# Performance work log

Hardware: AMD Instinct MI355X
Metric: run time of the kernel (lower is better)

The kernel has to match this reference:

```python
import jax, jax.numpy as jnp
import numpy as np
import math

B, S, DM = 32, 512, 1024   # batch (= groups*channels), seq_len, d_model
H, D, C = 16, 64, 8        # n_heads, d_kv, n_channels
NB, MD = 32, 128           # relative_attention_num_buckets, max_distance


def setup_inputs() -> dict:
    key = jax.random.key(0)
    ks = jax.random.split(key, 7)
    return {
        "hidden_states": jax.random.normal(ks[0], (B, S, DM), jnp.float32),
        "Wq": jax.random.normal(ks[1], (DM, H * D), jnp.float32) * 0.02,
        "Wk": jax.random.normal(ks[2], (DM, H * D), jnp.float32) * 0.02,
        "Wv": jax.random.normal(ks[3], (DM, H * D), jnp.float32) * 0.02,
        "Wo": jax.random.normal(ks[4], (H * D, DM), jnp.float32) * 0.02,
        "rel_emb": jax.random.normal(ks[5], (NB, H), jnp.float32) * 0.02,
        "beta": jax.random.normal(ks[6], (1, 1, H, 1, 1), jnp.float32) * 0.01,
    }


def _rel_bucket(relative_position, num_buckets=NB, max_distance=MD):
    # bidirectional (encoder) bucketing, faithful to T5
    nb = num_buckets // 2
    buckets = (relative_position > 0).astype(jnp.int32) * nb
    rp = jnp.abs(relative_position)
    max_exact = nb // 2
    is_small = rp < max_exact
    rp_safe = jnp.maximum(rp, 1).astype(jnp.float32)
    large = max_exact + (
        jnp.log(rp_safe / max_exact) / math.log(max_distance / max_exact) * (nb - max_exact)
    ).astype(jnp.int32)
    large = jnp.minimum(large, nb - 1)
    return buckets + jnp.where(is_small, rp, large)


def reference(hidden_states, Wq, Wk, Wv, Wo, rel_emb, beta):
    G = B // C  # groups

    def proj(W):
        # (B,S,DM) -> (B,S,H,D) -> (B,H,S,D) -> (G,C,H,S,D)
        x = (hidden_states @ W).reshape(B, S, H, D).transpose(0, 2, 1, 3)
        return x.reshape(G, C, H, S, D)

    q, k, v = proj(Wq), proj(Wk), proj(Wv)

    # relative position bias: (1,1,H,S,S)
    rel_pos = jnp.arange(S)[None, :] - jnp.arange(S)[:, None]
    bias = rel_emb[_rel_bucket(rel_pos)].transpose(2, 0, 1)[None, None]

    # local (dot-product) attention, T5-style: no 1/sqrt(d) scaling
    scores = jnp.einsum('gchsd,gchtd->gchst', q, k) + bias
    attn_w = jax.nn.softmax(scores, axis=-1)
    a_dot = jnp.einsum('gchst,gchtd->gchsd', attn_w, v)

    # compressive memory: ELU+1 feature map, summed over channels
    sk = jax.nn.elu(k) + 1.0
    M = jnp.einsum('gchsd,gchse->ghde', sk, v)   # (G,H,D,D)
    z = sk.sum(axis=3).sum(axis=1)               # (G,H,D)
    sq = jax.nn.elu(q) + 1.0
    num = jnp.einsum('gchsd,ghde->gchse', sq, M)
    den = jnp.einsum('gchsd,ghd->gchs', sq, z)[..., None] + 1e-6
    a_mem = num / den

    gate = jax.nn.sigmoid(beta)  # (1,1,H,1,1)
    out = gate * a_mem + (1.0 - gate) * a_dot

    # (G,C,H,S,D) -> (B,H,S,D) -> (B,S,H*D)
    out = out.reshape(B, H, S, D).transpose(0, 2, 1, 3).reshape(B, S, H * D)
    return out @ Wo
```

## Files before the change

### kernel.cpp

```cpp
#include <hip/hip_runtime.h>
#include <stdint.h>

typedef unsigned short u16;
typedef u16 u16x8 __attribute__((ext_vector_type(8)));
typedef u16 u16x4 __attribute__((ext_vector_type(4)));
typedef __bf16 bf16x8 __attribute__((ext_vector_type(8)));
typedef float f32x4 __attribute__((ext_vector_type(4)));

#define DEV static __device__ __forceinline__

DEV u16 f2bf(float f) {
  union { float f; uint32_t u; } v; v.f = f;
  uint32_t r = v.u + 0x7FFFu + ((v.u >> 16) & 1u);
  return (u16)(r >> 16);
}
DEV float bf2f(u16 s) {
  union { uint32_t u; float f; } v; v.u = ((uint32_t)s) << 16;
  return v.f;
}
DEV float elu1(float x) { return x > 0.f ? x + 1.f : __expf(x); }
DEV u16x8 ld8u(const u16* p) { return *reinterpret_cast<const u16x8*>(p); }

DEV f32x4 mfma16(u16x8 a, u16x8 b, f32x4 c) {
  return __builtin_amdgcn_mfma_f32_16x16x32_bf16(
      __builtin_bit_cast(bf16x8, a), __builtin_bit_cast(bf16x8, b), c, 0, 0, 0);
}
DEV void async16(void* lds, const void* g) {
  __builtin_amdgcn_global_load_lds(
      (__attribute__((address_space(1))) void*)g,
      (__attribute__((address_space(3))) void*)lds, 16, 0, 0);
}

#define BARR __builtin_amdgcn_s_barrier()
#define LG0  asm volatile("s_waitcnt lgkmcnt(0)" ::: "memory")
#define VMC(N) asm volatile("s_waitcnt vmcnt(" #N ")" ::: "memory")


__global__ __launch_bounds__(1024) void k_prep(const float* __restrict__ hs,
                                               const float* __restrict__ Wq, const float* __restrict__ Wk,
                                               const float* __restrict__ Wv, const float* __restrict__ Wo,
                                               const float* __restrict__ rel,
                                               u16* __restrict__ hsb, u16* __restrict__ wt,
                                               u16* __restrict__ wot, float* __restrict__ bias) {
  __shared__ float tb[32][33];
  const int blk = blockIdx.x;
  if (blk < 2048) {
    int i = blk * 1024 + threadIdx.x;
    const float4* p = reinterpret_cast<const float4*>(hs) + (size_t)i * 2;
    float4 a = p[0], bq = p[1];
    u16x8 o;
    o[0] = f2bf(a.x); o[1] = f2bf(a.y); o[2] = f2bf(a.z); o[3] = f2bf(a.w);
    o[4] = f2bf(bq.x); o[5] = f2bf(bq.y); o[6] = f2bf(bq.z); o[7] = f2bf(bq.w);
    reinterpret_cast<u16x8*>(hsb)[i] = o;
  } else if (blk < 6144) {
    const int bid2 = blk - 2048;
    int mat = bid2 >> 10;
    int tile = bid2 & 1023;
    int n0 = (tile >> 5) * 32;
    int k0 = (tile & 31) * 32;
    const float* W = (mat == 0) ? Wq : (mat == 1) ? Wk : (mat == 2) ? Wv : Wo;
    int tx = threadIdx.x & 31, ty = threadIdx.x >> 5;
    tb[ty][tx] = W[(size_t)(k0 + ty) * 1024 + n0 + tx];
    __syncthreads();
    u16 v = f2bf(tb[tx][ty]);
    if (mat < 3) wt[(size_t)(mat * 1024 + n0 + ty) * 1024 + k0 + tx] = v;
    else         wot[(size_t)(n0 + ty) * 1024 + k0 + tx] = v;
  } else {
    int off = threadIdx.x;
    if (off < 1023) {
      int rp = off - 511;
      int bck = rp > 0 ? 16 : 0;
      int arp = rp < 0 ? -rp : rp;
      int idx;
      if (arp < 8) idx = arp;
      else {
        float l = logf((float)arp * 0.125f) / logf(16.0f) * 8.0f;
        int lg = 8 + (int)l;
        idx = lg < 15 ? lg : 15;
      }
      bck += idx;
      for (int h = 0; h < 16; ++h) bias[h * 1023 + off] = rel[bck * 16 + h];
    }
  }
}


template <int EPI>
__global__ __launch_bounds__(512, 3) void k_g256(const u16* __restrict__ A, const u16* __restrict__ Bt,
                                                 u16* __restrict__ oq, u16* __restrict__ ok2,
                                                 u16* __restrict__ ovt, float* __restrict__ of) {
  __shared__ __align__(16) u16 lsA[2][128 * 32];
  __shared__ __align__(16) u16 lsB[2][256 * 32];
  const int t = threadIdx.x;
  const int lane = t & 63, w = t >> 6;
  const int wm = w >> 2, wn = w & 3;
  const int lr = lane & 15, lg = lane >> 4;

  const int bid = blockIdx.x;
  const int xcd = bid & 7, local = bid >> 3;
  const int s = local >> 4, w16 = local & 15;
  const int msq = s & 3, nsq = s >> 2;
  const int m0 = (xcd * 16 + msq * 4 + (w16 >> 2)) * 128;
  const int n0 = (nsq * 4 + (w16 & 3)) * 256;

  auto stage = [&](int kt, int slot) {
    const int k0 = kt * 32;
    {
      int c = t, S = c >> 3, q = (c & 7) ^ (S & 7);
      int row = 2 * S + (q >> 2), u = q & 3;
      async16(&lsA[slot][c * 8], A + (size_t)(m0 + row) * 1024 + k0 + u * 8);
    }
#pragma unroll
    for (int i = 0; i < 2; ++i) {
      int c = i * 512 + t, S = c >> 3, q = (c & 7) ^ (S & 7);
      int row = 2 * S + (q >> 2), u = q & 3;
      async16(&lsB[slot][c * 8], Bt + (size_t)(n0 + row) * 1024 + k0 + u * 8);
    }
  };
  auto rdoff = [&](int r_) -> int {
    return (r_ >> 1) * 64 + (((((r_ & 1) << 2) + lg) ^ ((r_ >> 1) & 7)) << 3);
  };

  f32x4 acc[4][4];
#pragma unroll
  for (int i = 0; i < 4; ++i)
#pragma unroll
    for (int j = 0; j < 4; ++j) acc[i][j] = (f32x4){0.f, 0.f, 0.f, 0.f};

  stage(0, 0);
  stage(1, 1);
  VMC(3);
  BARR;

  for (int kt = 0; kt < 32; ++kt) {
    const int slot = kt & 1;
    const u16* la = &lsA[slot][0];
    const u16* lb = &lsB[slot][0];

    u16x8 af[4], bf[4];
#pragma unroll
    for (int mi = 0; mi < 4; ++mi) af[mi] = ld8u(la + rdoff(wm * 64 + mi * 16 + lr));
#pragma unroll
    for (int ni = 0; ni < 4; ++ni) bf[ni] = ld8u(lb + rdoff(wn * 64 + ni * 16 + lr));
    LG0;
    BARR;
    if (kt + 2 < 32) stage(kt + 2, slot);

    __builtin_amdgcn_s_setprio(1);
#pragma unroll
    for (int mi = 0; mi < 4; ++mi)
#pragma unroll
      for (int ni = 0; ni < 4; ++ni)
        acc[mi][ni] = mfma16(af[mi], bf[ni], acc[mi][ni]);
    __builtin_amdgcn_s_setprio(0);

    if (kt + 2 < 32)      { VMC(3); }
    else if (kt == 30)    { VMC(0); }
    BARR;
  }

  if (EPI == 0) {
    const int which = n0 >> 10;
    const int nb = (n0 & 1023) + wn * 64;
#pragma unroll
    for (int mi = 0; mi < 4; ++mi)
#pragma unroll
      for (int r = 0; r < 4; ++r) {
        int m = m0 + wm * 64 + mi * 16 + lg * 4 + r;
        int b = m >> 9, s2 = m & 511;
#pragma unroll
        for (int ni = 0; ni < 4; ++ni) {
          int nc = nb + ni * 16 + lr;
          int h = nc >> 6, d = nc & 63;
          int bh = b * 16 + h;
          u16 v = f2bf(acc[mi][ni][r]);
          if (which == 0)      oq[(size_t)(bh * 512 + s2) * 64 + d] = v;
          else if (which == 1) ok2[(size_t)(bh * 512 + s2) * 64 + d] = v;
          else                 ovt[(size_t)(bh * 64 + d) * 512 + s2] = v;
        }
      }
  } else {
#pragma unroll
    for (int mi = 0; mi < 4; ++mi)
#pragma unroll
      for (int r = 0; r < 4; ++r) {
        int m = m0 + wm * 64 + mi * 16 + lg * 4 + r;
#pragma unroll
        for (int ni = 0; ni < 4; ++ni) {
          int n = n0 + wn * 64 + ni * 16 + lr;
          of[(size_t)m * 1024 + n] = acc[mi][ni][r];
        }
      }
  }
}


__global__ __launch_bounds__(256) void k_mem(const u16* __restrict__ K, const u16* __restrict__ Vt,
                                             float* __restrict__ Mp, float* __restrict__ zp) {
  __shared__ __align__(16) u16 skT[64 * 128];
  __shared__ __align__(16) u16 lV[64 * 128];
  __shared__ float mbuf[64][65];
  __shared__ float zsh[4][64];
  const int bid = blockIdx.x;
  const int g = bid >> 7, h = (bid >> 3) & 15, c = bid & 7;
  const int bh = (g * 8 + c) * 16 + h;
  const u16* kp = K + (size_t)bh * 512 * 64;
  const u16* vp = Vt + (size_t)bh * 64 * 512;
  const int t = threadIdx.x, lane = t & 63, w = t >> 6;
  const int lr = lane & 15, lg = lane >> 4;
  const int dmy = t & 63, sq = t >> 6;

  f32x4 acc[4][4];
#pragma unroll
  for (int i = 0; i < 4; ++i)
#pragma unroll
    for (int j = 0; j < 4; ++j) acc[i][j] = (f32x4){0.f, 0.f, 0.f, 0.f};
  float zacc = 0.f;

  for (int s0 = 0; s0 < 512; s0 += 128) {
#pragma unroll
    for (int i = 0; i < 4; ++i) {
      int c2 = i * 256 + t;
      int row = c2 >> 4, u = c2 & 15;
      async16(lV + c2 * 8, vp + (size_t)row * 512 + s0 + ((u ^ (row & 7)) << 3));
    }
#pragma unroll
    for (int r = 0; r < 4; ++r) {
      const int un = sq + r * 4;
      const int ss0 = un * 8;
      u16x8 vals;
#pragma unroll
      for (int j = 0; j < 8; ++j) {
        float x = elu1(bf2f(kp[(size_t)(s0 + ss0 + j) * 64 + dmy]));
        zacc += x;
        vals[j] = f2bf(x);
      }
      *reinterpret_cast<u16x8*>(skT + dmy * 128 + ((un ^ (dmy & 7)) << 3)) = vals;
    }
    VMC(0);
    __syncthreads();
    u16x8 af[4], bfv[4];
#pragma unroll
    for (int ds = 0; ds < 4; ++ds) {
      const int d = ds * 16 + lr;
      af[ds] = ld8u(skT + d * 128 + (((w * 4 + lg) ^ (d & 7)) << 3));
    }
#pragma unroll
    for (int es = 0; es < 4; ++es) {
      const int e = es * 16 + lr;
      bfv[es] = ld8u(lV + e * 128 + (((w * 4 + lg) ^ (e & 7)) << 3));
    }
#pragma unroll
    for (int ds = 0; ds < 4; ++ds)
#pragma unroll
      for (int es = 0; es < 4; ++es) acc[ds][es] = mfma16(af[ds], bfv[es], acc[ds][es]);
    __syncthreads();
  }

  zsh[sq][dmy] = zacc;
  for (int wv = 0; wv < 4; ++wv) {
    if (w == wv) {
#pragma unroll
      for (int ds = 0; ds < 4; ++ds)
#pragma unroll
        for (int es = 0; es < 4; ++es)
#pragma unroll
          for (int r = 0; r < 4; ++r) {
            int d = ds * 16 + lg * 4 + r, e = es * 16 + lr;
            if (wv == 0) mbuf[d][e] = acc[ds][es][r];
            else         mbuf[d][e] += acc[ds][es][r];
          }
    }
    __syncthreads();
  }
#pragma unroll
  for (int j = 0; j < 16; ++j) {
    int idx = j * 256 + t;
    Mp[(size_t)bid * 4096 + idx] = mbuf[idx >> 6][idx & 63];
  }
  if (t < 64) zp[(size_t)bid * 64 + t] = zsh[0][t] + zsh[1][t] + zsh[2][t] + zsh[3][t];
}

__global__ __launch_bounds__(256) void k_red(const float* __restrict__ Mp, const float* __restrict__ zp,
                                             u16* __restrict__ Mt, float* __restrict__ zv) {
  const int gh = blockIdx.x;
  const int t = threadIdx.x;
#pragma unroll
  for (int j = 0; j < 16; ++j) {
    int idx = j * 256 + t;
    int d = idx >> 6, e = idx & 63;
    float s = 0.f;
#pragma unroll
    for (int c = 0; c < 8; ++c) s += Mp[(size_t)(gh * 8 + c) * 4096 + idx];
    Mt[(size_t)gh * 4096 + e * 64 + d] = f2bf(s);
  }
  if (t < 64) {
    float s = 0.f;
#pragma unroll
    for (int c = 0; c < 8; ++c) s += zp[(size_t)(gh * 8 + c) * 64 + t];
    zv[gh * 64 + t] = s;
  }
}


__global__ __launch_bounds__(256, 3) void k_attn(const u16* __restrict__ Q, const u16* __restrict__ K,
                                                 const u16* __restrict__ Vt, const u16* __restrict__ Mt,
                                                 const float* __restrict__ zv, const float* __restrict__ bias,
                                                 const float* __restrict__ beta, u16* __restrict__ blend) {
  __shared__ __align__(16) u16 lK[2][64 * 64];
  __shared__ __align__(16) u16 lV[2][64 * 64];
  __shared__ __align__(16) u16 ps[4][32 * 64];
  __shared__ float lbias[640];
  __shared__ float zs[64];
  __shared__ float rsl[4][32];
  __shared__ float dnl[4][32];

  const int bid = blockIdx.x;
  const int vb = (bid & 7) * 256 + (bid >> 3);
  const int bh = vb >> 2, qg = vb & 3;
  const int b = bh >> 4, h = bh & 15, g = b >> 3;
  const int gh = g * 16 + h;
  const int t = threadIdx.x, lane = t & 63, w = t >> 6;
  const int lr = lane & 15, lg = lane >> 4;
  const int q0w = qg * 128 + w * 32;
  const u16* qp = Q + (size_t)bh * 512 * 64;
  const u16* kp = K + (size_t)bh * 512 * 64;
  const u16* vp = Vt + (size_t)bh * 64 * 512;
  const u16* mp = Mt + (size_t)gh * 4096;
  const float gate = 1.f / (1.f + __expf(-beta[h]));
  u16* psw = &ps[w][0];

  auto stage = [&](int kt, int sl) {
#pragma unroll
    for (int i = 0; i < 2; ++i) {
      int c = w * 128 + i * 64 + lane;
      int kr = c >> 3, u = c & 7;
      async16(&lK[sl][c * 8], kp + (size_t)(kt * 64 + kr) * 64 + ((u ^ (kr & 7)) << 3));
      async16(&lV[sl][c * 8], vp + (size_t)kr * 512 + kt * 64 + ((u ^ (kr & 7)) << 3));
    }
  };

  stage(0, 0);

  for (int i = t; i < 640; i += 256) lbias[i] = bias[h * 1023 + i + 384 - qg * 128];
  if (t < 64) zs[t] = zv[gh * 64 + t];
  LG0; BARR;

  u16x8 qf[2][2];
#pragma unroll
  for (int qs = 0; qs < 2; ++qs)
#pragma unroll
    for (int dc = 0; dc < 2; ++dc)
      qf[qs][dc] = ld8u(qp + (size_t)(q0w + qs * 16 + lr) * 64 + dc * 32 + lg * 8);

#pragma unroll
  for (int qs = 0; qs < 2; ++qs) {
    float sum = 0.f;
#pragma unroll
    for (int dc = 0; dc < 2; ++dc)
#pragma unroll
      for (int j = 0; j < 8; ++j)
        sum += elu1(bf2f(qf[qs][dc][j])) * zs[dc * 32 + lg * 8 + j];
    sum += __shfl_xor(sum, 16, 64);
    sum += __shfl_xor(sum, 32, 64);
    if (lane < 16) dnl[w][qs * 16 + lane] = sum + 1e-6f;
  }

  f32x4 acc[2][4];
#pragma unroll
  for (int qs = 0; qs < 2; ++qs)
#pragma unroll
    for (int es = 0; es < 4; ++es) acc[qs][es] = (f32x4){0.f, 0.f, 0.f, 0.f};
  float rs[2] = {0.f, 0.f};

  for (int kt = 0; kt < 8; ++kt) {
    const int sl = kt & 1;
    if (kt + 1 < 8) stage(kt + 1, sl ^ 1);
    if (kt + 1 < 8) { VMC(4); } else { VMC(0); }
    BARR;

#pragma unroll
    for (int ks = 0; ks < 4; ++ks) {
      const int kr = ks * 16 + lr;
      u16x8 kf0 = ld8u(&lK[sl][kr * 64 + (((0 * 4 + lg) ^ (kr & 7)) << 3)]);
      u16x8 kf1 = ld8u(&lK[sl][kr * 64 + (((1 * 4 + lg) ^ (kr & 7)) << 3)]);
#pragma unroll
      for (int qs = 0; qs < 2; ++qs) {
        f32x4 s = mfma16(kf0, qf[qs][0], (f32x4){0.f, 0.f, 0.f, 0.f});
        s = mfma16(kf1, qf[qs][1], s);
        const int bb = kt * 64 + ks * 16 + lg * 4 - (w * 32 + qs * 16 + lr) + 127;
        u16x4 pk;
        float lsum = 0.f;
#pragma unroll
        for (int r = 0; r < 4; ++r) {
          float p = __expf(s[r] + lbias[bb + r]);
          lsum += p;
          pk[r] = f2bf(p);
        }
        rs[qs] += lsum;
        const int row = qs * 16 + lr;
        const int addr = row * 64 + (((ks * 2 + (lg >> 1)) ^ (row & 7)) << 3) + (lg & 1) * 4;
        *reinterpret_cast<u16x4*>(psw + addr) = pk;
      }
    }
#pragma unroll
    for (int kc = 0; kc < 2; ++kc) {
      u16x8 pf[2];
#pragma unroll
      for (int qs = 0; qs < 2; ++qs) {
        const int row = qs * 16 + lr;
        pf[qs] = ld8u(psw + row * 64 + (((kc * 4 + lg) ^ (row & 7)) << 3));
      }
#pragma unroll
      for (int es = 0; es < 4; ++es) {
        const int er = es * 16 + lr;
        u16x8 vf = ld8u(&lV[sl][er * 64 + (((kc * 4 + lg) ^ (er & 7)) << 3)]);
#pragma unroll
        for (int qs = 0; qs < 2; ++qs) acc[qs][es] = mfma16(pf[qs], vf, acc[qs][es]);
      }
    }
    BARR;
  }

#pragma unroll
  for (int qs = 0; qs < 2; ++qs) {
    float v = rs[qs];
    v += __shfl_xor(v, 16, 64);
    v += __shfl_xor(v, 32, 64);
    if (lane < 16) rsl[w][qs * 16 + lane] = 1.f / v;
  }

  u16x8 sqf[2][2];
#pragma unroll
  for (int qs = 0; qs < 2; ++qs)
#pragma unroll
    for (int dc = 0; dc < 2; ++dc)
#pragma unroll
      for (int j = 0; j < 8; ++j) sqf[qs][dc][j] = f2bf(elu1(bf2f(qf[qs][dc][j])));
  f32x4 am[2][4];
#pragma unroll
  for (int qs = 0; qs < 2; ++qs)
#pragma unroll
    for (int es = 0; es < 4; ++es) am[qs][es] = (f32x4){0.f, 0.f, 0.f, 0.f};
#pragma unroll
  for (int es = 0; es < 4; ++es)
#pragma unroll
    for (int dc = 0; dc < 2; ++dc) {
      u16x8 mf = ld8u(mp + (es * 16 + lr) * 64 + dc * 32 + lg * 8);
#pragma unroll
      for (int qs = 0; qs < 2; ++qs) am[qs][es] = mfma16(sqf[qs][dc], mf, am[qs][es]);
    }

  u16* obuf = &ps[0][0];
#pragma unroll
  for (int qs = 0; qs < 2; ++qs)
#pragma unroll
    for (int r = 0; r < 4; ++r) {
      const int rowl = qs * 16 + lg * 4 + r;
      const int rowg = w * 32 + rowl;
      const float rinv = rsl[w][rowl];
      const float den = dnl[w][rowl];
#pragma unroll
      for (int es = 0; es < 4; ++es) {
        float o = gate * (am[qs][es][r] / den) + (1.f - gate) * acc[qs][es][r] * rinv;
        const int unit = es * 2 + (lr >> 3);
        obuf[rowg * 64 + ((unit ^ (rowg & 7)) << 3) + (lr & 7)] = f2bf(o);
      }
    }
  LG0; BARR;
  const int q0blk = qg * 128;
#pragma unroll
  for (int i = 0; i < 4; ++i) {
    const int row = w * 8 + i * 32 + (lane >> 3);
    const int un = lane & 7;
    u16x8 v = ld8u(obuf + row * 64 + ((un ^ (row & 7)) << 3));
    *reinterpret_cast<u16x8*>(blend + (size_t)(b * 512 + q0blk + row) * 1024 + h * 64 + un * 8) = v;
  }
}


extern "C" void kernel_launch(void* const* d_in, const int* in_sizes, int n_in,
                              void* d_out, int out_size, void* d_ws, size_t ws_size,
                              hipStream_t stream) {
  (void)in_sizes; (void)n_in; (void)out_size; (void)ws_size;
  const float* hs   = (const float*)d_in[0];
  const float* Wq   = (const float*)d_in[1];
  const float* Wk   = (const float*)d_in[2];
  const float* Wv   = (const float*)d_in[3];
  const float* Wo   = (const float*)d_in[4];
  const float* rel  = (const float*)d_in[5];
  const float* beta = (const float*)d_in[6];
  float* out = (float*)d_out;

  char* ws = (char*)d_ws;
  size_t off = 0;
  auto alloc = [&](size_t bytes) -> char* {
    char* p = ws + off;
    off += (bytes + 255) & ~(size_t)255;
    return p;
  };
  u16* hsb    = (u16*)alloc(16384ull * 1024 * 2);
  u16* wt     = (u16*)alloc(3072ull * 1024 * 2);
  u16* wot    = (u16*)alloc(1024ull * 1024 * 2);
  u16* q      = (u16*)alloc(16384ull * 1024 * 2);
  u16* k      = (u16*)alloc(16384ull * 1024 * 2);
  u16* vt     = (u16*)alloc(16384ull * 1024 * 2);
  float* Mp   = (float*)alloc(512ull * 4096 * 4);
  float* zp   = (float*)alloc(512ull * 64 * 4);
  u16* Mt     = (u16*)alloc(64ull * 4096 * 2);
  float* zv   = (float*)alloc(64ull * 64 * 4);
  float* bias = (float*)alloc(16ull * 1023 * 4);
  u16* blend  = hsb;

  k_prep<<<6145, 1024, 0, stream>>>(hs, Wq, Wk, Wv, Wo, rel, hsb, wt, wot, bias);
  k_g256<0><<<1536, 512, 0, stream>>>(hsb, wt, q, k, vt, nullptr);
  k_mem<<<512, 256, 0, stream>>>(k, vt, Mp, zp);
  k_red<<<64, 256, 0, stream>>>(Mp, zp, Mt, zv);
  k_attn<<<2048, 256, 0, stream>>>(q, k, vt, Mt, zv, bias, beta, blend);
  k_g256<1><<<512, 512, 0, stream>>>(blend, wot, nullptr, nullptr, nullptr, out);
}
```

Baseline: 331.7 us.

## Load GEMM B operand directly from global into registers, bypassing LDS

The 256-wide GEMM kernel no longer stages the B (weight) tile through shared memory. Each wave loads its B fragments straight from global memory into registers, one k-step ahead, alternating between two register sets in a manually unrolled loop. Only A still goes through LDS. This removes the B LDS writes and reads and frees 32KB of LDS per block. In exchange, each B tile is fetched separately by both wave rows. The per-lane global loads are also less coalesced (16 rows, 64B each), which adds L2 traffic and global-load latency on the critical path.

```diff
diff --git a/kernel.cpp b/kernel.cpp
--- a/kernel.cpp
+++ b/kernel.cpp
@@ -90,7 +90,6 @@
                                                  u16* __restrict__ oq, u16* __restrict__ ok2,
                                                  u16* __restrict__ ovt, float* __restrict__ of) {
   __shared__ __align__(16) u16 lsA[2][128 * 32];
-  __shared__ __align__(16) u16 lsB[2][256 * 32];
   const int t = threadIdx.x;
   const int lane = t & 63, w = t >> 6;
   const int wm = w >> 2, wn = w & 3;
@@ -103,23 +102,16 @@
   const int m0 = (xcd * 16 + msq * 4 + (w16 >> 2)) * 128;
   const int n0 = (nsq * 4 + (w16 & 3)) * 256;
 
-  auto stage = [&](int kt, int slot) {
+  auto stageA = [&](int kt, int slot) {
     const int k0 = kt * 32;
-    {
-      int c = t, S = c >> 3, q = (c & 7) ^ (S & 7);
-      int row = 2 * S + (q >> 2), u = q & 3;
-      async16(&lsA[slot][c * 8], A + (size_t)(m0 + row) * 1024 + k0 + u * 8);
-    }
-#pragma unroll
-    for (int i = 0; i < 2; ++i) {
-      int c = i * 512 + t, S = c >> 3, q = (c & 7) ^ (S & 7);
-      int row = 2 * S + (q >> 2), u = q & 3;
-      async16(&lsB[slot][c * 8], Bt + (size_t)(n0 + row) * 1024 + k0 + u * 8);
-    }
+    int c = t, S = c >> 3, q = (c & 7) ^ (S & 7);
+    int row = 2 * S + (q >> 2), u = q & 3;
+    async16(&lsA[slot][c * 8], A + (size_t)(m0 + row) * 1024 + k0 + u * 8);
   };
   auto rdoff = [&](int r_) -> int {
     return (r_ >> 1) * 64 + (((((r_ & 1) << 2) + lg) ^ ((r_ >> 1) & 7)) << 3);
   };
+  const u16* pB = Bt + (size_t)(n0 + wn * 64 + lr) * 1024 + lg * 8;
 
   f32x4 acc[4][4];
 #pragma unroll
@@ -127,37 +119,44 @@
 #pragma unroll
     for (int j = 0; j < 4; ++j) acc[i][j] = (f32x4){0.f, 0.f, 0.f, 0.f};
 
-  stage(0, 0);
-  stage(1, 1);
-  VMC(3);
+  u16x8 bA[4], bB[4];
+
+  stageA(0, 0);
+  stageA(1, 1);
+#pragma unroll
+  for (int ni = 0; ni < 4; ++ni) bA[ni] = ld8u(pB + (size_t)ni * 16384);
+  VMC(5);
   BARR;
 
-  for (int kt = 0; kt < 32; ++kt) {
-    const int slot = kt & 1;
-    const u16* la = &lsA[slot][0];
-    const u16* lb = &lsB[slot][0];
-
-    u16x8 af[4], bf[4];
-#pragma unroll
-    for (int mi = 0; mi < 4; ++mi) af[mi] = ld8u(la + rdoff(wm * 64 + mi * 16 + lr));
-#pragma unroll
-    for (int ni = 0; ni < 4; ++ni) bf[ni] = ld8u(lb + rdoff(wn * 64 + ni * 16 + lr));
-    LG0;
-    BARR;
-    if (kt + 2 < 32) stage(kt + 2, slot);
-
-    __builtin_amdgcn_s_setprio(1);
-#pragma unroll
-    for (int mi = 0; mi < 4; ++mi)
-#pragma unroll
-      for (int ni = 0; ni < 4; ++ni)
-        acc[mi][ni] = mfma16(af[mi], bf[ni], acc[mi][ni]);
-    __builtin_amdgcn_s_setprio(0);
-
-    if (kt + 2 < 32)      { VMC(3); }
-    else if (kt == 30)    { VMC(0); }
-    BARR;
-  }
+#define GITER(KT, SLOT, BCUR, BNX)                                            \
+  {                                                                           \
+    const u16* la = &lsA[SLOT][0];                                            \
+    u16x8 af[4];                                                              \
+    _Pragma("unroll") for (int mi = 0; mi < 4; ++mi)                          \
+        af[mi] = ld8u(la + rdoff(wm * 64 + mi * 16 + lr));                    \
+    if ((KT) + 1 < 32) {                                                      \
+      _Pragma("unroll") for (int ni = 0; ni < 4; ++ni)                        \
+          BNX[ni] = ld8u(pB + ((KT) + 1) * 32 + (size_t)ni * 16384);          \
+    }                                                                         \
+    LG0;                                                                      \
+    BARR;                                                                     \
+    if ((KT) + 2 < 32) stageA((KT) + 2, SLOT);                                \
+    __builtin_amdgcn_s_setprio(1);                                            \
+    _Pragma("unroll") for (int mi = 0; mi < 4; ++mi)                          \
+    _Pragma("unroll") for (int ni = 0; ni < 4; ++ni)                          \
+        acc[mi][ni] = mfma16(af[mi], BCUR[ni], acc[mi][ni]);                  \
+    __builtin_amdgcn_s_setprio(0);                                            \
+    if ((KT) + 2 < 32)      { VMC(5); }                                       \
+    else if ((KT) == 30)    { VMC(4); }                                       \
+    BARR;                                                                     \
+  }
+
+  for (int kt2 = 0; kt2 < 16; ++kt2) {
+    const int kt = kt2 * 2;
+    GITER(kt, 0, bA, bB);
+    GITER(kt + 1, 1, bB, bA);
+  }
+#undef GITER
 
   if (EPI == 0) {
     const int which = n0 >> 10;
```

New measurement: 509.5 us. 53.6% more time.
